# Optimization experiments

Measured on AMD Instinct MI355X. Metric: run time of the kernel, lower is better.

## Reference

```python
import jax, jax.numpy as jnp
import numpy as np

D_MODEL = 1024
NUM_HEADS = 16
HEAD_DIM = D_MODEL // NUM_HEADS


def setup_inputs() -> dict:
    key = jax.random.key(0)
    ks = jax.random.split(key, 11)
    B, S = 2, 2048
    scale = 1.0 / np.sqrt(D_MODEL)
    inp = {
        "q": jax.random.normal(ks[0], (B, S, D_MODEL), jnp.float32),
        "k": jax.random.normal(ks[1], (B, S, D_MODEL), jnp.float32),
        "v": jax.random.normal(ks[2], (B, S, D_MODEL), jnp.float32),
        "Wq": jax.random.normal(ks[3], (D_MODEL, D_MODEL), jnp.float32) * scale,
        "bq": jnp.zeros((D_MODEL,), jnp.float32),
        "Wk": jax.random.normal(ks[4], (D_MODEL, D_MODEL), jnp.float32) * scale,
        "bk": jnp.zeros((D_MODEL,), jnp.float32),
        "Wv": jax.random.normal(ks[5], (D_MODEL, D_MODEL), jnp.float32) * scale,
        "bv": jnp.zeros((D_MODEL,), jnp.float32),
        "Wo": jax.random.normal(ks[6], (D_MODEL, D_MODEL), jnp.float32) * scale,
        "bo": jnp.zeros((D_MODEL,), jnp.float32),
    }
    return inp


def reference(q, k, v, Wq, bq, Wk, bk, Wv, bv, Wo, bo):
    B, S, _ = q.shape
    # Linear projections (torch Linear: x @ W.T + b), split into heads -> [b,h,s,d]
    def proj(x, W, b):
        y = jnp.einsum('bsm,nm->bsn', x, W) + b
        return y.reshape(B, -1, NUM_HEADS, HEAD_DIM).transpose(0, 2, 1, 3)
    qh = proj(q, Wq, bq)
    kh = proj(k, Wk, bk)
    vh = proj(v, Wv, bv)
    # NOTE: source scales by sqrt(d_model), NOT sqrt(head_dim) -- faithful quirk
    factor = jnp.sqrt(jnp.float32(D_MODEL))
    scores = jnp.einsum('bhqd,bhkd->bhqk', qh, kh) / factor
    attn = jax.nn.softmax(scores, axis=-1)
    out = jnp.einsum('bhqk,bhkd->bhqd', attn, vh)
    out = out.transpose(0, 2, 1, 3).reshape(B, S, D_MODEL)
    # out projection; dropout=0.0 (eval) is identity
    return jnp.einsum('bsm,nm->bsn', out, Wo) + bo
```

## Files before the change

### kernel.cpp

```cpp
#include <hip/hip_runtime.h>
#include <hip/hip_bf16.h>

typedef __hip_bfloat16 bf16;
typedef short short8 __attribute__((ext_vector_type(8)));
typedef short bs4 __attribute__((ext_vector_type(4)));
typedef float f32x4 __attribute__((ext_vector_type(4)));
typedef float f32x16 __attribute__((ext_vector_type(16)));

#define MFMA_BF16(a, b, c) __builtin_amdgcn_mfma_f32_16x16x32_bf16(a, b, c, 0, 0, 0)
#define MFMA32_BF16(a, b, c) __builtin_amdgcn_mfma_f32_32x32x16_bf16(a, b, c, 0, 0, 0)

#define QSCALE 0.045084439f

__device__ __forceinline__ void async_copy16(const bf16* g, bf16* l) {
    __builtin_amdgcn_global_load_lds(
        (const __attribute__((address_space(1))) unsigned int*)(const void*)g,
        (__attribute__((address_space(3))) unsigned int*)(void*)l, 16, 0, 0);
}

__global__ __launch_bounds__(256) void convert_all(
    const float* __restrict__ q, const float* __restrict__ k, const float* __restrict__ v,
    const float* __restrict__ wq, const float* __restrict__ wk,
    const float* __restrict__ wv, const float* __restrict__ wo,
    bf16* __restrict__ qb, bf16* __restrict__ kb, bf16* __restrict__ vb,
    bf16* __restrict__ wqb, bf16* __restrict__ wkb, bf16* __restrict__ wvb,
    bf16* __restrict__ wob)
{
    int blk = blockIdx.x;
    const float* s; bf16* d; int rel;
    if      (blk < 1024) { s = q;  d = qb;  rel = blk; }
    else if (blk < 2048) { s = k;  d = kb;  rel = blk - 1024; }
    else if (blk < 3072) { s = v;  d = vb;  rel = blk - 2048; }
    else if (blk < 3328) { s = wq; d = wqb; rel = blk - 3072; }
    else if (blk < 3584) { s = wk; d = wkb; rel = blk - 3328; }
    else if (blk < 3840) { s = wv; d = wvb; rel = blk - 3584; }
    else                 { s = wo; d = wob; rel = blk - 3840; }
    size_t base = (size_t)rel * 1024 + threadIdx.x;
#pragma unroll
    for (int i = 0; i < 4; i++) {
        float4 f = ((const float4*)s)[base + i * 256];
        union { bf16 h[4]; uint2 u; } pk;
        pk.h[0] = (bf16)f.x; pk.h[1] = (bf16)f.y;
        pk.h[2] = (bf16)f.z; pk.h[3] = (bf16)f.w;
        ((uint2*)d)[base + i * 256] = pk.u;
    }
}

__global__ __launch_bounds__(256) void gemm_qkv(
    const bf16* __restrict__ qb, const bf16* __restrict__ kb, const bf16* __restrict__ vb,
    const bf16* __restrict__ wqb, const bf16* __restrict__ wkb, const bf16* __restrict__ wvb,
    const float* __restrict__ bq, const float* __restrict__ bk, const float* __restrict__ bv,
    bf16* __restrict__ Qp, bf16* __restrict__ Kp, bf16* __restrict__ Vt)
{
    __shared__ bf16 Al[2][128 * 64];
    __shared__ bf16 Bl[2][128 * 64];

    const int sel = blockIdx.y >> 3;
    const bf16* A; const bf16* W; const float* bias;
    if      (sel == 0) { A = qb; W = wqb; bias = bq; }
    else if (sel == 1) { A = kb; W = wkb; bias = bk; }
    else               { A = vb; W = wvb; bias = bv; }

    const int K = 1024, N = 1024;
    const int t = threadIdx.x;
    const int lane = t & 63, wave = t >> 6;
    const int ln = lane & 15, quad = lane >> 4;
    const int wm = wave >> 1, wn = wave & 1;
    const int m0 = blockIdx.x * 128, n0 = (blockIdx.y & 7) * 128;

    f32x4 acc[4][4];
#pragma unroll
    for (int i = 0; i < 4; i++)
#pragma unroll
        for (int j = 0; j < 4; j++) acc[i][j] = (f32x4){0.f, 0.f, 0.f, 0.f};

    const int lk = ln & 7;
    const int srow = t >> 3, sidx0 = t & 7;

#define STAGE_AB(buf_, k0_) do {                                               \
    const bf16* Ab = A + (size_t)m0 * K + (k0_);                               \
    const bf16* Wb = W + (size_t)n0 * K + (k0_);                               \
    _Pragma("unroll")                                                          \
    for (int p = 0; p < 4; p++) {                                              \
        int row = p * 32 + srow, idx = sidx0 ^ (row & 7);                      \
        async_copy16(Ab + (size_t)row * K + idx * 8,                           \
                     &Al[buf_][(p * 256 + wave * 64) * 8]);                    \
    }                                                                          \
    _Pragma("unroll")                                                          \
    for (int p = 0; p < 4; p++) {                                              \
        int row = p * 32 + srow, idx = sidx0 ^ (row & 7);                      \
        async_copy16(Wb + (size_t)row * K + idx * 8,                           \
                     &Bl[buf_][(p * 256 + wave * 64) * 8]);                    \
    }                                                                          \
} while (0)

    STAGE_AB(0, 0);

    for (int k0 = 0; k0 < K; k0 += 64) {
        const int cur = (k0 >> 6) & 1;
        if (k0 < K - 64) {
            STAGE_AB(cur ^ 1, k0 + 64);
            asm volatile("s_waitcnt vmcnt(8)" ::: "memory");
        } else {
            asm volatile("s_waitcnt vmcnt(0)" ::: "memory");
        }
        __builtin_amdgcn_s_barrier();

        const bf16* Alc = Al[cur];
        const bf16* Blc = Bl[cur];

#pragma unroll
        for (int kk = 0; kk < 2; kk++) {
            short8 af[4], bfr[4];
#pragma unroll
            for (int i = 0; i < 4; i++) {
                int r = wm * 64 + i * 16 + ln;
                af[i] = *(const short8*)&Alc[r * 64 + (((kk << 2) | quad) ^ lk) * 8];
            }
#pragma unroll
            for (int j = 0; j < 4; j++) {
                int r = wn * 64 + j * 16 + ln;
                bfr[j] = *(const short8*)&Blc[r * 64 + (((kk << 2) | quad) ^ lk) * 8];
            }
            __builtin_amdgcn_s_setprio(1);
#pragma unroll
            for (int i = 0; i < 4; i++)
#pragma unroll
                for (int j = 0; j < 4; j++)
                    acc[i][j] = MFMA_BF16(af[i], bfr[j], acc[i][j]);
            __builtin_amdgcn_s_setprio(0);
        }

        asm volatile("" ::: "memory");
        __builtin_amdgcn_s_barrier();
    }
#undef STAGE_AB

#pragma unroll
    for (int j = 0; j < 4; j++) {
        int c = n0 + wn * 64 + j * 16 + ln;
        float bv2 = bias[c];
        if (sel == 2) {
            int h = c >> 6, dd = c & 63;
#pragma unroll
            for (int i = 0; i < 4; i++) {
                int m = m0 + wm * 64 + i * 16 + quad * 4;
                int bb = m >> 11, s = m & 2047;
                union { bf16 h4[4]; uint2 u; } pk;
#pragma unroll
                for (int r = 0; r < 4; r++) pk.h4[r] = (bf16)(acc[i][j][r] + bv2);
                *(uint2*)&Vt[(((size_t)(bb * 16 + h)) * 64 + dd) * 2048 + s] = pk.u;
            }
        } else {
            bf16* out = (sel == 0) ? Qp : Kp;
            float scl = (sel == 0) ? QSCALE : 1.0f;
#pragma unroll
            for (int i = 0; i < 4; i++) {
                int rb = m0 + wm * 64 + i * 16 + quad * 4;
#pragma unroll
                for (int r = 0; r < 4; r++)
                    out[(size_t)(rb + r) * N + c] = (bf16)((acc[i][j][r] + bv2) * scl);
            }
        }
    }
}

__global__ __launch_bounds__(256) void gemm_fin(
    const bf16* __restrict__ A, const bf16* __restrict__ W,
    const float* __restrict__ bias, float* __restrict__ C)
{
    __shared__ bf16 Al[2][128 * 64];
    __shared__ bf16 Bl[2][64 * 64];

    const int K = 1024, N = 1024;
    const int t = threadIdx.x;
    const int lane = t & 63, wave = t >> 6;
    const int ln = lane & 15, quad = lane >> 4;
    const int wm = wave >> 1, wn = wave & 1;
    const int m0 = blockIdx.x * 128, n0 = blockIdx.y * 64;

    f32x4 acc[4][2];
#pragma unroll
    for (int i = 0; i < 4; i++)
#pragma unroll
        for (int j = 0; j < 2; j++) acc[i][j] = (f32x4){0.f, 0.f, 0.f, 0.f};

    const int lk = ln & 7;
    const int srow = t >> 3, sidx0 = t & 7;

#define STAGE_AB(buf_, k0_) do {                                               \
    const bf16* Ab = A + (size_t)m0 * K + (k0_);                               \
    const bf16* Wb = W + (size_t)n0 * K + (k0_);                               \
    _Pragma("unroll")                                                          \
    for (int p = 0; p < 4; p++) {                                              \
        int row = p * 32 + srow, idx = sidx0 ^ (row & 7);                      \
        async_copy16(Ab + (size_t)row * K + idx * 8,                           \
                     &Al[buf_][(p * 256 + wave * 64) * 8]);                    \
    }                                                                          \
    _Pragma("unroll")                                                          \
    for (int p = 0; p < 2; p++) {                                              \
        int row = p * 32 + srow, idx = sidx0 ^ (row & 7);                      \
        async_copy16(Wb + (size_t)row * K + idx * 8,                           \
                     &Bl[buf_][(p * 256 + wave * 64) * 8]);                    \
    }                                                                          \
} while (0)

    STAGE_AB(0, 0);

    for (int k0 = 0; k0 < K; k0 += 64) {
        const int cur = (k0 >> 6) & 1;
        if (k0 < K - 64) {
            STAGE_AB(cur ^ 1, k0 + 64);
            asm volatile("s_waitcnt vmcnt(6)" ::: "memory");
        } else {
            asm volatile("s_waitcnt vmcnt(0)" ::: "memory");
        }
        __builtin_amdgcn_s_barrier();

        const bf16* Alc = Al[cur];
        const bf16* Blc = Bl[cur];

#pragma unroll
        for (int kk = 0; kk < 2; kk++) {
            short8 af[4], bfr[2];
#pragma unroll
            for (int i = 0; i < 4; i++) {
                int r = wm * 64 + i * 16 + ln;
                af[i] = *(const short8*)&Alc[r * 64 + (((kk << 2) | quad) ^ lk) * 8];
            }
#pragma unroll
            for (int j = 0; j < 2; j++) {
                int r = wn * 32 + j * 16 + ln;
                bfr[j] = *(const short8*)&Blc[r * 64 + (((kk << 2) | quad) ^ lk) * 8];
            }
            __builtin_amdgcn_s_setprio(1);
#pragma unroll
            for (int i = 0; i < 4; i++)
#pragma unroll
                for (int j = 0; j < 2; j++)
                    acc[i][j] = MFMA_BF16(af[i], bfr[j], acc[i][j]);
            __builtin_amdgcn_s_setprio(0);
        }

        asm volatile("" ::: "memory");
        __builtin_amdgcn_s_barrier();
    }
#undef STAGE_AB

#pragma unroll
    for (int j = 0; j < 2; j++) {
        int c = n0 + wn * 32 + j * 16 + ln;
        float bv2 = bias[c];
#pragma unroll
        for (int i = 0; i < 4; i++) {
            int rb = m0 + wm * 64 + i * 16 + quad * 4;
#pragma unroll
            for (int r = 0; r < 4; r++)
                C[(size_t)(rb + r) * N + c] = acc[i][j][r] + bv2;
        }
    }
}

__global__ __launch_bounds__(512, 4) void attn128q(
    const bf16* __restrict__ Q, const bf16* __restrict__ K,
    const bf16* __restrict__ V, bf16* __restrict__ O)
{
    const int S = 2048, D = 1024;
    __shared__ bf16 Kl[2][128 * 64];
    __shared__ bf16 Vl[2][64 * 128];

    const int t = threadIdx.x, lane = t & 63, wave = t >> 6;
    const int lo = lane & 31, hi = lane >> 5;
    const int keyhalf = wave >> 2;
    const int qw = wave & 3;
    const int h = blockIdx.x & 15, b = blockIdx.x >> 4, qt = blockIdx.y;
    const size_t kqbase = (size_t)b * S * D + (size_t)h * 64;
    const size_t vbase = ((size_t)(b * 16 + h)) * 64 * 2048;

    const int q0 = qt * 128 + qw * 32;
    short8 aq[4];
    {
        const bf16* qp = Q + kqbase + (size_t)(q0 + lo) * D + hi * 8;
#pragma unroll
        for (int s = 0; s < 4; s++) aq[s] = *(const short8*)(qp + s * 16);
    }
    asm volatile("" :: "v"(aq[0]), "v"(aq[1]), "v"(aq[2]), "v"(aq[3]));

    f32x16 o0, o1, ol;
#pragma unroll
    for (int i = 0; i < 16; i++) { o0[i] = 0.f; o1[i] = 0.f; ol[i] = 0.f; }

    const short8 vones = (short8)(short)0x3F80;

    int koff[4];
#pragma unroll
    for (int s = 0; s < 4; s++)
        koff[s] = lo * 64 + (((2 * s + hi) ^ (lo & 7)) * 8);
    const int khbase = keyhalf * 64 * 64;

    const int x0 = (keyhalf * 8) ^ (lo & 15);
    const int vbl = lo * 128 + hi * 4;

    const int krow = t >> 3, kidx = t & 7;
    const int vrow = t >> 4, vidx = t & 15;

#define STAGE_KV(buf_, kt_) do {                                               \
    _Pragma("unroll")                                                          \
    for (int p = 0; p < 2; p++) {                                              \
        int row = p * 64 + krow, idx = kidx ^ (row & 7);                       \
        async_copy16(K + kqbase + (size_t)((kt_) * 128 + row) * D + idx * 8,   \
                     &Kl[buf_][(p * 512 + wave * 64) * 8]);                    \
    }                                                                          \
    _Pragma("unroll")                                                          \
    for (int p = 0; p < 2; p++) {                                              \
        int row = p * 32 + vrow, idx = vidx ^ (row & 15);                      \
        async_copy16(V + vbase + (size_t)row * 2048 + (kt_) * 128 + idx * 8,   \
                     &Vl[buf_][(p * 512 + wave * 64) * 8]);                    \
    }                                                                          \
} while (0)

    STAGE_KV(0, 0);

    for (int kt = 0; kt < S / 128; kt++) {
        const int cur = kt & 1;
        if (kt < S / 128 - 1) {
            STAGE_KV(cur ^ 1, kt + 1);
            asm volatile("s_waitcnt vmcnt(4)" ::: "memory");
        } else {
            asm volatile("s_waitcnt vmcnt(0)" ::: "memory");
        }
        __builtin_amdgcn_s_barrier();

        const bf16* Klc = Kl[cur];
        const bf16* Vlc = Vl[cur];

#pragma unroll
        for (int kg = 0; kg < 2; kg++) {
            const bf16* kb = Klc + khbase + kg * (32 * 64);
            short8 kf0 = *(const short8*)(kb + koff[0]);
            short8 kf1 = *(const short8*)(kb + koff[1]);
            short8 kf2 = *(const short8*)(kb + koff[2]);
            short8 kf3 = *(const short8*)(kb + koff[3]);

            __builtin_amdgcn_s_setprio(1);
            f32x16 acc;
#pragma unroll
            for (int i = 0; i < 16; i++) acc[i] = 0.f;
            acc = MFMA32_BF16(kf0, aq[0], acc);
            acc = MFMA32_BF16(kf1, aq[1], acc);
            acc = MFMA32_BF16(kf2, aq[2], acc);
            acc = MFMA32_BF16(kf3, aq[3], acc);
            __builtin_amdgcn_s_setprio(0);

            union { bf16 hh[8]; short8 s; } pk0, pk1;
#pragma unroll
            for (int r = 0; r < 8; r++)
                pk0.hh[r] = (bf16)__builtin_amdgcn_exp2f(acc[r]);
#pragma unroll
            for (int r = 0; r < 8; r++)
                pk1.hh[r] = (bf16)__builtin_amdgcn_exp2f(acc[8 + r]);

            __builtin_amdgcn_s_setprio(1);
            ol = MFMA32_BF16(pk0.s, vones, ol);
            ol = MFMA32_BF16(pk1.s, vones, ol);
#pragma unroll
            for (int db = 0; db < 2; db++) {
#pragma unroll
                for (int c = 0; c < 2; c++) {
                    const int m = kg * 4 + 2 * c;
                    union { bs4 hh[2]; short8 s; } vf;
                    vf.hh[0] = *(const bs4*)&Vlc[vbl + db * 4096 + ((x0 ^ m) * 8)];
                    vf.hh[1] = *(const bs4*)&Vlc[vbl + db * 4096 + ((x0 ^ (m + 1)) * 8)];
                    if (db == 0) o0 = MFMA32_BF16(c ? pk1.s : pk0.s, vf.s, o0);
                    else         o1 = MFMA32_BF16(c ? pk1.s : pk0.s, vf.s, o1);
                }
            }
            __builtin_amdgcn_s_setprio(0);
        }

        asm volatile("" ::: "memory");
        __builtin_amdgcn_s_barrier();
    }
#undef STAGE_KV

    float* os = (float*)&Kl[0][0];
    float* ls = (float*)&Vl[0][0];
    if (wave >= 4) {
        const int w4 = wave - 4;
#pragma unroll
        for (int i = 0; i < 16; i++) os[(w4 * 32 + i) * 64 + lane] = o0[i];
#pragma unroll
        for (int i = 0; i < 16; i++) os[(w4 * 32 + 16 + i) * 64 + lane] = o1[i];
#pragma unroll
        for (int i = 0; i < 16; i++) ls[(w4 * 16 + i) * 64 + lane] = ol[i];
    }
    __syncthreads();
    if (wave < 4) {
#pragma unroll
        for (int i = 0; i < 16; i++) o0[i] += os[(wave * 32 + i) * 64 + lane];
#pragma unroll
        for (int i = 0; i < 16; i++) o1[i] += os[(wave * 32 + 16 + i) * 64 + lane];
#pragma unroll
        for (int i = 0; i < 16; i++) ol[i] += ls[(wave * 16 + i) * 64 + lane];
#pragma unroll
        for (int r = 0; r < 16; r++) {
            float invr = __builtin_amdgcn_rcpf(ol[r]);
            const int q = (r & 3) + 8 * (r >> 2) + 4 * hi;
            const int row = qt * 128 + qw * 32 + q;
            bf16* op = O + ((size_t)b * S + row) * D + h * 64 + lo;
            op[0]  = (bf16)(o0[r] * invr);
            op[32] = (bf16)(o1[r] * invr);
        }
    }
}

extern "C" void kernel_launch(void* const* d_in, const int* in_sizes, int n_in,
                              void* d_out, int out_size, void* d_ws, size_t ws_size,
                              hipStream_t stream) {
    (void)in_sizes; (void)n_in; (void)out_size; (void)ws_size;
    const float* q  = (const float*)d_in[0];
    const float* k  = (const float*)d_in[1];
    const float* v  = (const float*)d_in[2];
    const float* Wq = (const float*)d_in[3];
    const float* bq = (const float*)d_in[4];
    const float* Wk = (const float*)d_in[5];
    const float* bk = (const float*)d_in[6];
    const float* Wv = (const float*)d_in[7];
    const float* bv = (const float*)d_in[8];
    const float* Wo = (const float*)d_in[9];
    const float* bo = (const float*)d_in[10];
    float* out = (float*)d_out;

    const int M = 4096, N = 1024;
    const size_t MN = (size_t)M * N;
    const size_t NN = (size_t)N * N;
    bf16* qb  = (bf16*)d_ws;
    bf16* kb  = qb + MN;
    bf16* vb  = kb + MN;
    bf16* wqb = vb + MN;
    bf16* wkb = wqb + NN;
    bf16* wvb = wkb + NN;
    bf16* wob = wvb + NN;
    bf16* Qp  = wob + NN;
    bf16* Kp  = Qp + MN;
    bf16* Vt  = Kp + MN;
    bf16* AO  = qb;

    dim3 blk(256);
    convert_all<<<4096, blk, 0, stream>>>(q, k, v, Wq, Wk, Wv, Wo,
                                          qb, kb, vb, wqb, wkb, wvb, wob);

    gemm_qkv<<<dim3(32, 24), blk, 0, stream>>>(qb, kb, vb, wqb, wkb, wvb,
                                               bq, bk, bv, Qp, Kp, Vt);

    attn128q<<<dim3(32, 16), dim3(512), 0, stream>>>(Qp, Kp, Vt, AO);

    gemm_fin<<<dim3(32, 16), blk, 0, stream>>>(AO, wob, bo, out);
}
```

Measured before the change: 211.6 us.

## Fuse fp32-to-bf16 activation conversion into the QKV GEMM tile loads

```diff
diff --git a/kernel.cpp b/kernel.cpp
--- a/kernel.cpp
+++ b/kernel.cpp
@@ -18,23 +18,20 @@
         (__attribute__((address_space(3))) unsigned int*)(void*)l, 16, 0, 0);
 }
 
-__global__ __launch_bounds__(256) void convert_all(
-    const float* __restrict__ q, const float* __restrict__ k, const float* __restrict__ v,
+__global__ __launch_bounds__(256) void convert_w(
     const float* __restrict__ wq, const float* __restrict__ wk,
     const float* __restrict__ wv, const float* __restrict__ wo,
-    bf16* __restrict__ qb, bf16* __restrict__ kb, bf16* __restrict__ vb,
     bf16* __restrict__ wqb, bf16* __restrict__ wkb, bf16* __restrict__ wvb,
     bf16* __restrict__ wob)
 {
     int blk = blockIdx.x;
-    const float* s; bf16* d; int rel;
-    if      (blk < 1024) { s = q;  d = qb;  rel = blk; }
-    else if (blk < 2048) { s = k;  d = kb;  rel = blk - 1024; }
-    else if (blk < 3072) { s = v;  d = vb;  rel = blk - 2048; }
-    else if (blk < 3328) { s = wq; d = wqb; rel = blk - 3072; }
-    else if (blk < 3584) { s = wk; d = wkb; rel = blk - 3328; }
-    else if (blk < 3840) { s = wv; d = wvb; rel = blk - 3584; }
-    else                 { s = wo; d = wob; rel = blk - 3840; }
+    const float* s; bf16* d; int rel = blk & 255;
+    switch (blk >> 8) {
+        case 0:  s = wq; d = wqb; break;
+        case 1:  s = wk; d = wkb; break;
+        case 2:  s = wv; d = wvb; break;
+        default: s = wo; d = wob; break;
+    }
     size_t base = (size_t)rel * 1024 + threadIdx.x;
 #pragma unroll
     for (int i = 0; i < 4; i++) {
@@ -47,7 +44,7 @@
 }
 
 __global__ __launch_bounds__(256) void gemm_qkv(
-    const bf16* __restrict__ qb, const bf16* __restrict__ kb, const bf16* __restrict__ vb,
+    const float* __restrict__ qf, const float* __restrict__ kf, const float* __restrict__ vf_,
     const bf16* __restrict__ wqb, const bf16* __restrict__ wkb, const bf16* __restrict__ wvb,
     const float* __restrict__ bq, const float* __restrict__ bk, const float* __restrict__ bv,
     bf16* __restrict__ Qp, bf16* __restrict__ Kp, bf16* __restrict__ Vt)
@@ -56,10 +53,10 @@
     __shared__ bf16 Bl[2][128 * 64];
 
     const int sel = blockIdx.y >> 3;
-    const bf16* A; const bf16* W; const float* bias;
-    if      (sel == 0) { A = qb; W = wqb; bias = bq; }
-    else if (sel == 1) { A = kb; W = wkb; bias = bk; }
-    else               { A = vb; W = wvb; bias = bv; }
+    const float* A; const bf16* W; const float* bias;
+    if      (sel == 0) { A = qf;  W = wqb; bias = bq; }
+    else if (sel == 1) { A = kf;  W = wkb; bias = bk; }
+    else               { A = vf_; W = wvb; bias = bv; }
 
     const int K = 1024, N = 1024;
     const int t = threadIdx.x;
@@ -77,15 +74,34 @@
     const int lk = ln & 7;
     const int srow = t >> 3, sidx0 = t & 7;
 
-#define STAGE_AB(buf_, k0_) do {                                               \
-    const bf16* Ab = A + (size_t)m0 * K + (k0_);                               \
-    const bf16* Wb = W + (size_t)n0 * K + (k0_);                               \
+    float4 ar[8];
+
+#define LOAD_A(k0_) do {                                                       \
+    const float* Af = A + (size_t)m0 * K + (k0_);                              \
     _Pragma("unroll")                                                          \
     for (int p = 0; p < 4; p++) {                                              \
         int row = p * 32 + srow, idx = sidx0 ^ (row & 7);                      \
-        async_copy16(Ab + (size_t)row * K + idx * 8,                           \
-                     &Al[buf_][(p * 256 + wave * 64) * 8]);                    \
-    }                                                                          \
+        const float* src = Af + (size_t)row * K + idx * 8;                     \
+        ar[2 * p]     = *(const float4*)(src);                                 \
+        ar[2 * p + 1] = *(const float4*)(src + 4);                             \
+    }                                                                          \
+} while (0)
+
+#define WRITE_A(buf_) do {                                                     \
+    _Pragma("unroll")                                                          \
+    for (int p = 0; p < 4; p++) {                                              \
+        int row = p * 32 + srow;                                               \
+        union { bf16 h[8]; short8 s; } cv;                                     \
+        cv.h[0] = (bf16)ar[2 * p].x;     cv.h[1] = (bf16)ar[2 * p].y;          \
+        cv.h[2] = (bf16)ar[2 * p].z;     cv.h[3] = (bf16)ar[2 * p].w;          \
+        cv.h[4] = (bf16)ar[2 * p + 1].x; cv.h[5] = (bf16)ar[2 * p + 1].y;      \
+        cv.h[6] = (bf16)ar[2 * p + 1].z; cv.h[7] = (bf16)ar[2 * p + 1].w;      \
+        *(short8*)&Al[buf_][row * 64 + sidx0 * 8] = cv.s;                      \
+    }                                                                          \
+} while (0)
+
+#define STAGE_B(buf_, k0_) do {                                                \
+    const bf16* Wb = W + (size_t)n0 * K + (k0_);                               \
     _Pragma("unroll")                                                          \
     for (int p = 0; p < 4; p++) {                                              \
         int row = p * 32 + srow, idx = sidx0 ^ (row & 7);                      \
@@ -94,16 +110,21 @@
     }                                                                          \
 } while (0)
 
-    STAGE_AB(0, 0);
+    LOAD_A(0);
+    STAGE_B(0, 0);
+    asm volatile("s_waitcnt vmcnt(4)" ::: "memory");
+    WRITE_A(0);
 
     for (int k0 = 0; k0 < K; k0 += 64) {
         const int cur = (k0 >> 6) & 1;
         if (k0 < K - 64) {
-            STAGE_AB(cur ^ 1, k0 + 64);
-            asm volatile("s_waitcnt vmcnt(8)" ::: "memory");
+            LOAD_A(k0 + 64);
+            STAGE_B(cur ^ 1, k0 + 64);
+            asm volatile("s_waitcnt vmcnt(12)" ::: "memory");
         } else {
             asm volatile("s_waitcnt vmcnt(0)" ::: "memory");
         }
+        asm volatile("s_waitcnt lgkmcnt(0)" ::: "memory");
         __builtin_amdgcn_s_barrier();
 
         const bf16* Alc = Al[cur];
@@ -131,10 +152,16 @@
             __builtin_amdgcn_s_setprio(0);
         }
 
-        asm volatile("" ::: "memory");
-        __builtin_amdgcn_s_barrier();
-    }
-#undef STAGE_AB
+        if (k0 < K - 64) {
+            asm volatile("s_waitcnt vmcnt(4)" ::: "memory");
+            WRITE_A(cur ^ 1);
+        }
+        asm volatile("s_waitcnt lgkmcnt(0)" ::: "memory");
+        __builtin_amdgcn_s_barrier();
+    }
+#undef LOAD_A
+#undef WRITE_A
+#undef STAGE_B
 
 #pragma unroll
     for (int j = 0; j < 4; j++) {
@@ -447,10 +474,9 @@
     bf16* AO  = qb;
 
     dim3 blk(256);
-    convert_all<<<4096, blk, 0, stream>>>(q, k, v, Wq, Wk, Wv, Wo,
-                                          qb, kb, vb, wqb, wkb, wvb, wob);
-
-    gemm_qkv<<<dim3(32, 24), blk, 0, stream>>>(qb, kb, vb, wqb, wkb, wvb,
+    convert_w<<<1024, blk, 0, stream>>>(Wq, Wk, Wv, Wo, wqb, wkb, wvb, wob);
+
+    gemm_qkv<<<dim3(32, 24), blk, 0, stream>>>(q, k, v, wqb, wkb, wvb,
                                                bq, bk, bv, Qp, Kp, Vt);
 
     attn128q<<<dim3(32, 16), dim3(512), 0, stream>>>(Qp, Kp, Vt, AO);
```

Result: slower. 221.0 us (+4.4%).
